# Performance work log

Measured on AMD Instinct MI355X. Metric: run time of the kernel, lower is better.

Reference implementation:

```python
import jax, jax.numpy as jnp
import numpy as np

H = 1024
B, S = 4, 2048
SCALE = 1.0 / np.sqrt(H)  # single-head: head_dim == hidden_dim


def setup_inputs() -> dict:
    key = jax.random.key(0)
    k1, k2, k3, k4 = jax.random.split(key, 4)
    inp = jax.random.normal(k1, (B, S, H), dtype=jnp.float32)
    # nn.Linear(h, h, bias=False) weights, stored [out, in]
    wq = jax.random.normal(k2, (H, H), dtype=jnp.float32) / np.sqrt(H)
    wk = jax.random.normal(k3, (H, H), dtype=jnp.float32) / np.sqrt(H)
    wv = jax.random.normal(k4, (H, H), dtype=jnp.float32) / np.sqrt(H)
    # causal mask, broadcast over batch: 1 = attend, 0 = masked
    attention_mask = jnp.broadcast_to(
        jnp.tril(jnp.ones((S, S), dtype=jnp.int32)), (B, S, S))
    return {"input": inp, "attention_mask": attention_mask,
            "wq": wq, "wk": wk, "wv": wv}


def reference(input, attention_mask, wq, wk, wv):
    # Linear: x @ W^T
    Q = jnp.einsum('bsh,oh->bso', input, wq)
    K = jnp.einsum('bsh,oh->bso', input, wk)
    V = jnp.einsum('bsh,oh->bso', input, wv)
    scores = jnp.einsum('bqh,bkh->bqk', Q, K) * SCALE  # [B,S,S]
    neg_inf = jnp.asarray(-jnp.inf, dtype=scores.dtype)
    scores = jnp.where(attention_mask == 0, neg_inf, scores)
    attn = jax.nn.softmax(scores, axis=-1)
    # dropout prob = 0.0 (eval): identity
    return jnp.einsum('bqk,bkh->bqh', attn, V)
```

## Files before the change

### kernel.cpp

```cpp
#include <hip/hip_runtime.h>
#include <hip/hip_bf16.h>
#include <stdint.h>

typedef __attribute__((ext_vector_type(8))) short short8;
typedef __attribute__((ext_vector_type(4))) float f32x4;
typedef __attribute__((ext_vector_type(4))) float fvec4;
typedef __attribute__((ext_vector_type(4))) unsigned short us4;

#define DEV static __device__ __forceinline__

constexpr int Hn = 1024;
constexpr int Bn = 4;
constexpr int Sn = 2048;
constexpr float SCALE_F = 0.03125f;
constexpr float LOG2E_F = 1.4426950408889634f;
constexpr float CEXP = SCALE_F * LOG2E_F;

DEV unsigned short f2bf(float f) {
  union { float f; unsigned u; } c; c.f = f;
  unsigned r = c.u + 0x7fffu + ((c.u >> 16) & 1u);
  return (unsigned short)(r >> 16);
}

DEV float bf2f(unsigned short b) {
  union { unsigned u; float f; } c; c.u = ((unsigned)b) << 16;
  return c.f;
}

DEV void gload16(const void* g, void* l) {
  __builtin_amdgcn_global_load_lds(
      (const __attribute__((address_space(1))) void*)g,
      (__attribute__((address_space(3))) void*)l, 16, 0, 0);
}

__global__ __launch_bounds__(256) void cvt_kernel(
    const float* __restrict__ x, const float* __restrict__ wq,
    const float* __restrict__ wk, const float* __restrict__ wv,
    unsigned short* __restrict__ xb, unsigned short* __restrict__ wb) {
  const int NX4 = Bn * Sn * Hn / 4;
  const int NW4 = Hn * Hn / 4;
  const int total = NX4 + 3 * NW4;
  for (int i = blockIdx.x * 256 + threadIdx.x; i < total; i += gridDim.x * 256) {
    const fvec4* s; us4* d; int j;
    if (i < NX4)                { s = (const fvec4*)x;  d = (us4*)xb;             j = i; }
    else if (i < NX4 + NW4)     { s = (const fvec4*)wq; d = (us4*)wb;             j = i - NX4; }
    else if (i < NX4 + 2 * NW4) { s = (const fvec4*)wk; d = (us4*)(wb + Hn * Hn); j = i - NX4 - NW4; }
    else                        { s = (const fvec4*)wv; d = (us4*)(wb + 2 * Hn * Hn); j = i - NX4 - 2 * NW4; }
    fvec4 v = s[j];
    us4 o;
    o[0] = f2bf(v[0]); o[1] = f2bf(v[1]); o[2] = f2bf(v[2]); o[3] = f2bf(v[3]);
    d[j] = o;
  }
}

__global__ __launch_bounds__(256) void gemm_bt_dbuf_kernel(
    const unsigned short* __restrict__ A, int lda,
    const unsigned short* __restrict__ Bm, int ldb,
    unsigned short* __restrict__ C0, unsigned short* __restrict__ C1,
    int n_split, int ldc, int bm_mask, int bm_shift, int K) {
  __shared__ __attribute__((aligned(16))) unsigned short As[2][128 * 32];
  __shared__ __attribute__((aligned(16))) unsigned short Bs[2][128 * 32];
  const int tid = threadIdx.x, lane = tid & 63, wave = tid >> 6;
  const int wr = wave >> 1, wc = wave & 1;
  const int q8 = gridDim.x >> 3;
  const int wgid = (blockIdx.x & 7) * q8 + (blockIdx.x >> 3);
  const int bm = wgid & bm_mask, bn = wgid >> bm_shift;

  const unsigned short* Ag = A + (int64_t)(bm * 128 + wave * 32 + (lane >> 2)) * lda + (lane & 3) * 8;
  const unsigned short* Bg = Bm + (int64_t)(bn * 128 + wave * 32 + (lane >> 2)) * ldb + (lane & 3) * 8;

  f32x4 zero = {0.f, 0.f, 0.f, 0.f};
  f32x4 acc[4][4];
#pragma unroll
  for (int m = 0; m < 4; m++)
#pragma unroll
    for (int n = 0; n < 4; n++) acc[m][n] = zero;

  auto stage = [&](int kt, int buf) {
    const int k0 = kt << 5;
    char* a = (char*)As[buf] + wave * 2048;
    char* b = (char*)Bs[buf] + wave * 2048;
    gload16(Ag + k0, a);
    gload16(Ag + k0 + 16 * lda, a + 1024);
    gload16(Bg + k0, b);
    gload16(Bg + k0 + 16 * ldb, b + 1024);
  };

  const int nkt = K >> 5;
  stage(0, 0);
  __syncthreads();
  for (int kt = 0; kt < nkt; ++kt) {
    const int buf = kt & 1;
    if (kt + 1 < nkt) stage(kt + 1, buf ^ 1);
    const short* Ap = (const short*)As[buf];
    const short* Bp = (const short*)Bs[buf];
    const int ko = (lane >> 4) * 8;
    short8 af[4], bfv[4];
#pragma unroll
    for (int m = 0; m < 4; m++)
      af[m] = *(const short8*)(Ap + (wr * 64 + m * 16 + (lane & 15)) * 32 + ko);
#pragma unroll
    for (int n = 0; n < 4; n++)
      bfv[n] = *(const short8*)(Bp + (wc * 64 + n * 16 + (lane & 15)) * 32 + ko);
#pragma unroll
    for (int m = 0; m < 4; m++)
#pragma unroll
      for (int n = 0; n < 4; n++)
        acc[m][n] = __builtin_amdgcn_mfma_f32_16x16x32_bf16(af[m], bfv[n], acc[m][n], 0, 0, 0);
    __syncthreads();
  }

#pragma unroll
  for (int n = 0; n < 4; n++) {
    int cc = bn * 128 + wc * 64 + n * 16;
    unsigned short* cb = C0;
    if (cc >= n_split) { cb = C1; cc -= n_split; }
    cc += (lane & 15);
#pragma unroll
    for (int m = 0; m < 4; m++) {
      const int r0 = bm * 128 + wr * 64 + m * 16 + ((lane >> 4) << 2);
#pragma unroll
      for (int j = 0; j < 4; j++)
        cb[(int64_t)(r0 + j) * ldc + cc] = f2bf(acc[m][n][j]);
    }
  }
}

__global__ __launch_bounds__(256) void scores_exp_kernel(
    const unsigned short* __restrict__ Qb, const unsigned short* __restrict__ Kbuf,
    unsigned short* __restrict__ P, int64_t p_zstride, int b0) {
  const int q8 = gridDim.x >> 3;
  const int wgid = (blockIdx.x & 7) * q8 + (blockIdx.x >> 3);
  const int zl = wgid / 136;
  const int t = wgid - zl * 136;
  int bm = (int)((sqrtf(8.f * t + 1.f) - 1.f) * 0.5f);
  if (bm * (bm + 1) / 2 > t) bm--;
  if ((bm + 1) * (bm + 2) / 2 <= t) bm++;
  const int bn = t - bm * (bm + 1) / 2;

  const int b = b0 + zl;
  const unsigned short* A = Qb + (int64_t)b * Sn * Hn;
  const unsigned short* Bm = Kbuf + (int64_t)b * Sn * Hn;
  unsigned short* C = P + (int64_t)zl * p_zstride;

  __shared__ __attribute__((aligned(16))) unsigned short As[2][128 * 32];
  __shared__ __attribute__((aligned(16))) unsigned short Bs[2][128 * 32];
  const int tid = threadIdx.x, lane = tid & 63, wave = tid >> 6;
  const int wr = wave >> 1, wc = wave & 1;

  const unsigned short* Ag = A + (int64_t)(bm * 128 + wave * 32 + (lane >> 2)) * Hn + (lane & 3) * 8;
  const unsigned short* Bg = Bm + (int64_t)(bn * 128 + wave * 32 + (lane >> 2)) * Hn + (lane & 3) * 8;

  f32x4 zero = {0.f, 0.f, 0.f, 0.f};
  f32x4 acc[4][4];
#pragma unroll
  for (int m = 0; m < 4; m++)
#pragma unroll
    for (int n = 0; n < 4; n++) acc[m][n] = zero;

  auto stage = [&](int kt, int buf) {
    const int k0 = kt << 5;
    char* a = (char*)As[buf] + wave * 2048;
    char* b2 = (char*)Bs[buf] + wave * 2048;
    gload16(Ag + k0, a);
    gload16(Ag + k0 + 16 * Hn, a + 1024);
    gload16(Bg + k0, b2);
    gload16(Bg + k0 + 16 * Hn, b2 + 1024);
  };

  stage(0, 0);
  __syncthreads();
  for (int kt = 0; kt < (Hn >> 5); ++kt) {
    const int buf = kt & 1;
    if (kt + 1 < (Hn >> 5)) stage(kt + 1, buf ^ 1);
    const short* Ap = (const short*)As[buf];
    const short* Bp = (const short*)Bs[buf];
    const int ko = (lane >> 4) * 8;
    short8 af[4], bfv[4];
#pragma unroll
    for (int m = 0; m < 4; m++)
      af[m] = *(const short8*)(Ap + (wr * 64 + m * 16 + (lane & 15)) * 32 + ko);
#pragma unroll
    for (int n = 0; n < 4; n++)
      bfv[n] = *(const short8*)(Bp + (wc * 64 + n * 16 + (lane & 15)) * 32 + ko);
#pragma unroll
    for (int m = 0; m < 4; m++)
#pragma unroll
      for (int n = 0; n < 4; n++)
        acc[m][n] = __builtin_amdgcn_mfma_f32_16x16x32_bf16(af[m], bfv[n], acc[m][n], 0, 0, 0);
    __syncthreads();
  }

#pragma unroll
  for (int n = 0; n < 4; n++) {
    const int cc = bn * 128 + wc * 64 + n * 16 + (lane & 15);
#pragma unroll
    for (int m = 0; m < 4; m++) {
      const int r0 = bm * 128 + wr * 64 + m * 16 + ((lane >> 4) << 2);
#pragma unroll
      for (int j = 0; j < 4; j++) {
        const int row = r0 + j;
        const float p = (cc <= row) ? __builtin_amdgcn_exp2f(acc[m][n][j] * CEXP) : 0.f;
        C[(int64_t)row * Sn + cc] = f2bf(p);
      }
    }
  }
}

__global__ __launch_bounds__(256) void rowsum_kernel(
    const unsigned short* __restrict__ P, float* __restrict__ l, int b0, int nb) {
  const int lane = threadIdx.x & 63, wave = threadIdx.x >> 6;
  const int r = blockIdx.x * 4 + wave;
  if (r >= nb * Sn) return;
  const int bl = r >> 11;
  const int q = r & (Sn - 1);
  const unsigned short* Pr = P + (int64_t)bl * Sn * Sn + (int64_t)q * Sn;
  float s = 0.f;
  for (int base = lane * 8; base < Sn; base += 512) {
    const int rem = q + 1 - base;
    if (rem <= 0) continue;
    short8 v = *(const short8*)(Pr + base);
#pragma unroll
    for (int e = 0; e < 8; ++e)
      if (e < rem) s += bf2f((unsigned short)v[e]);
  }
#pragma unroll
  for (int m = 1; m < 64; m <<= 1) s += __shfl_xor(s, m);
  if (lane == 0) l[(int64_t)(b0 + bl) * Sn + q] = s;
}

__global__ __launch_bounds__(256) void pv_gemm_kernel(
    const unsigned short* __restrict__ P, int64_t p_zstride,
    const unsigned short* __restrict__ VTb,
    const float* __restrict__ l,
    float* __restrict__ Out, int b0, int nb) {
  const int per_bm = 8 * nb;
  const int w = blockIdx.x;
  const int bm = 15 - (w / per_bm);
  const int inner = w - (15 - bm) * per_bm;
  const int bn = inner & 7;
  const int zl = inner >> 3;
  const int b = b0 + zl;

  __shared__ __attribute__((aligned(16))) unsigned short As[2][128 * 32];
  __shared__ __attribute__((aligned(16))) unsigned short Bs[2][128 * 32];
  const int tid = threadIdx.x, lane = tid & 63, wave = tid >> 6;
  const int wr = wave >> 1, wc = wave & 1;

  const unsigned short* A = P + (int64_t)zl * p_zstride;
  const unsigned short* Ag = A + (int64_t)(bm * 128 + wave * 32 + (lane >> 2)) * Sn + (lane & 3) * 8;
  const unsigned short* Bg = VTb + (int64_t)(bn * 128 + wave * 32 + (lane >> 2)) * (Bn * Sn)
                             + (int64_t)b * Sn + (lane & 3) * 8;

  f32x4 zero = {0.f, 0.f, 0.f, 0.f};
  f32x4 acc[4][4];
#pragma unroll
  for (int m = 0; m < 4; m++)
#pragma unroll
    for (int n = 0; n < 4; n++) acc[m][n] = zero;

  auto stage = [&](int kt, int buf) {
    const int k0 = kt << 5;
    char* a = (char*)As[buf] + wave * 2048;
    char* b2 = (char*)Bs[buf] + wave * 2048;
    gload16(Ag + k0, a);
    gload16(Ag + k0 + 16 * Sn, a + 1024);
    gload16(Bg + k0, b2);
    gload16(Bg + k0 + (int64_t)16 * (Bn * Sn), b2 + 1024);
  };

  const int nkt = (bm + 1) * 4;
  stage(0, 0);
  __syncthreads();
  for (int kt = 0; kt < nkt; ++kt) {
    const int buf = kt & 1;
    if (kt + 1 < nkt) stage(kt + 1, buf ^ 1);
    const short* Ap = (const short*)As[buf];
    const short* Bp = (const short*)Bs[buf];
    const int ko = (lane >> 4) * 8;
    short8 af[4], bfv[4];
#pragma unroll
    for (int m = 0; m < 4; m++)
      af[m] = *(const short8*)(Ap + (wr * 64 + m * 16 + (lane & 15)) * 32 + ko);
#pragma unroll
    for (int n = 0; n < 4; n++)
      bfv[n] = *(const short8*)(Bp + (wc * 64 + n * 16 + (lane & 15)) * 32 + ko);
#pragma unroll
    for (int m = 0; m < 4; m++)
#pragma unroll
      for (int n = 0; n < 4; n++)
        acc[m][n] = __builtin_amdgcn_mfma_f32_16x16x32_bf16(af[m], bfv[n], acc[m][n], 0, 0, 0);
    __syncthreads();
  }

#pragma unroll
  for (int m = 0; m < 4; m++) {
    const int r0 = bm * 128 + wr * 64 + m * 16 + ((lane >> 4) << 2);
#pragma unroll
    for (int j = 0; j < 4; j++) {
      const int q = r0 + j;
      const float linv = 1.0f / l[(int64_t)b * Sn + q];
#pragma unroll
      for (int n = 0; n < 4; n++) {
        const int d = bn * 128 + wc * 64 + n * 16 + (lane & 15);
        Out[(int64_t)b * Sn * Hn + (int64_t)q * Hn + d] = acc[m][n][j] * linv;
      }
    }
  }
}

extern "C" void kernel_launch(void* const* d_in, const int* in_sizes, int n_in,
                              void* d_out, int out_size, void* d_ws, size_t ws_size,
                              hipStream_t stream) {
  const float* x  = (const float*)d_in[0];
  const float* wq = (const float*)d_in[2];
  const float* wk = (const float*)d_in[3];
  const float* wv = (const float*)d_in[4];
  float* out = (float*)d_out;
  char* ws = (char*)d_ws;

  const int64_t MiB = 1ll << 20;
  unsigned short* xb = (unsigned short*)(ws);
  unsigned short* wb = (unsigned short*)(ws + 16 * MiB);
  float* l           = (float*)(ws + 22 * MiB);
  unsigned short* Qb = (unsigned short*)(ws + 23 * MiB);
  unsigned short* Kb = (unsigned short*)(ws + 39 * MiB);
  unsigned short* VT = (unsigned short*)(ws + 55 * MiB);
  unsigned short* P  = (unsigned short*)(ws + 71 * MiB);

  cvt_kernel<<<2048, 256, 0, stream>>>(x, wq, wk, wv, xb, wb);
  gemm_bt_dbuf_kernel<<<1024, 256, 0, stream>>>(
      xb, 1024, wb, 1024, Qb, Kb, 1024, 1024, 63, 6, 1024);
  gemm_bt_dbuf_kernel<<<512, 256, 0, stream>>>(
      wb + 2 * 1024 * 1024, 1024, xb, 1024, VT, VT, 1 << 30, 8192, 7, 3, 1024);

  int nb = 1;
  if (ws_size >= 103ull * MiB) nb = 4;
  else if (ws_size >= 87ull * MiB) nb = 2;
  for (int b0 = 0; b0 < Bn; b0 += nb) {
    scores_exp_kernel<<<136 * nb, 256, 0, stream>>>(
        Qb, Kb, P, (int64_t)Sn * Sn, b0);
    rowsum_kernel<<<nb * 512, 256, 0, stream>>>(P, l, b0, nb);
    pv_gemm_kernel<<<16 * 8 * nb, 256, 0, stream>>>(
        P, (int64_t)Sn * Sn, VT, l, out, b0, nb);
  }
}
```

Measured before the change: 179.6 us.

## Replace 128x128 GEMM kernels with a unified 256x256-tile MFMA kernel using swizzled LDS

Replaces the projection GEMM and the causal scores+exp kernel with one templated kernel. It uses 256x256 output tiles, 512 threads, a K-step of 64 and XOR-swizzled LDS layout to avoid bank conflicts. It also adds explicit s_barrier/vmcnt double-buffer synchronisation, setprio around the MFMA bursts, and a remainder-aware XCD block swizzle. The larger tiles raise data reuse per LDS/global load. The cost is far fewer workgroups (128–256 per launch on a 256-CU part), 128KB of LDS per block, and more wasted work on diagonal causal tiles.

Measured after the change: 181.6 us. Within noise of the previous version (+1.1%).

```diff
diff --git a/kernel.cpp b/kernel.cpp
--- a/kernel.cpp
+++ b/kernel.cpp
@@ -31,6 +31,13 @@
   __builtin_amdgcn_global_load_lds(
       (const __attribute__((address_space(1))) void*)g,
       (__attribute__((address_space(3))) void*)l, 16, 0, 0);
+}
+
+DEV void hw_barrier() { asm volatile("s_barrier" ::: "memory"); }
+
+DEV int swz_wg(int bid, int n) {
+  const int q = n >> 3, r = n & 7, x = bid & 7, o = bid >> 3;
+  return (x < r ? x * (q + 1) : r * (q + 1) + (x - r) * q) + o;
 }
 
 __global__ __launch_bounds__(256) void cvt_kernel(
@@ -53,155 +60,136 @@
   }
 }
 
-__global__ __launch_bounds__(256) void gemm_bt_dbuf_kernel(
-    const unsigned short* __restrict__ A, int lda,
-    const unsigned short* __restrict__ Bm, int ldb,
+template <int MODE>
+__global__ __launch_bounds__(512, 2) void gemm256_kernel(
+    const unsigned short* __restrict__ A, int lda, int64_t a_bstride,
+    const unsigned short* __restrict__ Bm, int ldb, int64_t b_bstride,
     unsigned short* __restrict__ C0, unsigned short* __restrict__ C1,
-    int n_split, int ldc, int bm_mask, int bm_shift, int K) {
-  __shared__ __attribute__((aligned(16))) unsigned short As[2][128 * 32];
-  __shared__ __attribute__((aligned(16))) unsigned short Bs[2][128 * 32];
+    int n_split, int ldc, int64_t c_bstride, int bm_mod, int K) {
+  __shared__ __attribute__((aligned(16))) unsigned short LA[2][256 * 64];
+  __shared__ __attribute__((aligned(16))) unsigned short LB[2][256 * 64];
   const int tid = threadIdx.x, lane = tid & 63, wave = tid >> 6;
-  const int wr = wave >> 1, wc = wave & 1;
-  const int q8 = gridDim.x >> 3;
-  const int wgid = (blockIdx.x & 7) * q8 + (blockIdx.x >> 3);
-  const int bm = wgid & bm_mask, bn = wgid >> bm_shift;
-
-  const unsigned short* Ag = A + (int64_t)(bm * 128 + wave * 32 + (lane >> 2)) * lda + (lane & 3) * 8;
-  const unsigned short* Bg = Bm + (int64_t)(bn * 128 + wave * 32 + (lane >> 2)) * ldb + (lane & 3) * 8;
+  const int wr = wave >> 2, wc = wave & 3;
+
+  int bm, bn;
+  const unsigned short* Ab = A;
+  const unsigned short* Bb = Bm;
+  unsigned short* Cb = C0;
+  if (MODE == 0) {
+    const int wg = swz_wg(blockIdx.x, gridDim.x);
+    bm = wg % bm_mod;
+    bn = wg / bm_mod;
+  } else {
+    const int wg = swz_wg(blockIdx.x, gridDim.x);
+    const int zl = wg / 36;
+    const int t = wg - zl * 36;
+    bm = (int)((sqrtf(8.f * t + 1.f) - 1.f) * 0.5f);
+    if (bm * (bm + 1) / 2 > t) bm--;
+    if ((bm + 1) * (bm + 2) / 2 <= t) bm++;
+    bn = t - bm * (bm + 1) / 2;
+    Ab += (int64_t)zl * a_bstride;
+    Bb += (int64_t)zl * b_bstride;
+    Cb += (int64_t)zl * c_bstride;
+  }
+
+  const int srow = wave * 32 + (lane >> 3);
+  const int scol = (((lane & 7) ^ (lane >> 3)) << 3);
+  const unsigned short* AgS = Ab + (int64_t)(bm * 256 + srow) * lda + scol;
+  const unsigned short* BgS = Bb + (int64_t)(bn * 256 + srow) * ldb + scol;
 
   f32x4 zero = {0.f, 0.f, 0.f, 0.f};
-  f32x4 acc[4][4];
-#pragma unroll
-  for (int m = 0; m < 4; m++)
+  f32x4 acc[8][4];
+#pragma unroll
+  for (int m = 0; m < 8; m++)
 #pragma unroll
     for (int n = 0; n < 4; n++) acc[m][n] = zero;
 
-  auto stage = [&](int kt, int buf) {
-    const int k0 = kt << 5;
-    char* a = (char*)As[buf] + wave * 2048;
-    char* b = (char*)Bs[buf] + wave * 2048;
-    gload16(Ag + k0, a);
-    gload16(Ag + k0 + 16 * lda, a + 1024);
-    gload16(Bg + k0, b);
-    gload16(Bg + k0 + 16 * ldb, b + 1024);
+  auto stage = [&](int t, int buf) {
+    char* la = (char*)LA[buf] + wave * 4096;
+    char* lb = (char*)LB[buf] + wave * 4096;
+    const int k0 = t << 6;
+#pragma unroll
+    for (int j = 0; j < 4; ++j) {
+      gload16(AgS + (int64_t)(j * 8) * lda + k0, la + j * 1024);
+      gload16(BgS + (int64_t)(j * 8) * ldb + k0, lb + j * 1024);
+    }
   };
 
-  const int nkt = K >> 5;
+  const int nkt = K >> 6;
+  const int ln15 = lane & 15;
+  const int hi = (lane >> 4) * 16;
+  const int sw = (ln15 & 7) << 4;
+
   stage(0, 0);
-  __syncthreads();
-  for (int kt = 0; kt < nkt; ++kt) {
-    const int buf = kt & 1;
-    if (kt + 1 < nkt) stage(kt + 1, buf ^ 1);
-    const short* Ap = (const short*)As[buf];
-    const short* Bp = (const short*)Bs[buf];
-    const int ko = (lane >> 4) * 8;
-    short8 af[4], bfv[4];
-#pragma unroll
-    for (int m = 0; m < 4; m++)
-      af[m] = *(const short8*)(Ap + (wr * 64 + m * 16 + (lane & 15)) * 32 + ko);
-#pragma unroll
-    for (int n = 0; n < 4; n++)
-      bfv[n] = *(const short8*)(Bp + (wc * 64 + n * 16 + (lane & 15)) * 32 + ko);
-#pragma unroll
-    for (int m = 0; m < 4; m++)
-#pragma unroll
-      for (int n = 0; n < 4; n++)
-        acc[m][n] = __builtin_amdgcn_mfma_f32_16x16x32_bf16(af[m], bfv[n], acc[m][n], 0, 0, 0);
-    __syncthreads();
-  }
-
-#pragma unroll
-  for (int n = 0; n < 4; n++) {
-    int cc = bn * 128 + wc * 64 + n * 16;
-    unsigned short* cb = C0;
-    if (cc >= n_split) { cb = C1; cc -= n_split; }
-    cc += (lane & 15);
-#pragma unroll
-    for (int m = 0; m < 4; m++) {
-      const int r0 = bm * 128 + wr * 64 + m * 16 + ((lane >> 4) << 2);
-#pragma unroll
-      for (int j = 0; j < 4; j++)
-        cb[(int64_t)(r0 + j) * ldc + cc] = f2bf(acc[m][n][j]);
-    }
-  }
-}
-
-__global__ __launch_bounds__(256) void scores_exp_kernel(
-    const unsigned short* __restrict__ Qb, const unsigned short* __restrict__ Kbuf,
-    unsigned short* __restrict__ P, int64_t p_zstride, int b0) {
-  const int q8 = gridDim.x >> 3;
-  const int wgid = (blockIdx.x & 7) * q8 + (blockIdx.x >> 3);
-  const int zl = wgid / 136;
-  const int t = wgid - zl * 136;
-  int bm = (int)((sqrtf(8.f * t + 1.f) - 1.f) * 0.5f);
-  if (bm * (bm + 1) / 2 > t) bm--;
-  if ((bm + 1) * (bm + 2) / 2 <= t) bm++;
-  const int bn = t - bm * (bm + 1) / 2;
-
-  const int b = b0 + zl;
-  const unsigned short* A = Qb + (int64_t)b * Sn * Hn;
-  const unsigned short* Bm = Kbuf + (int64_t)b * Sn * Hn;
-  unsigned short* C = P + (int64_t)zl * p_zstride;
-
-  __shared__ __attribute__((aligned(16))) unsigned short As[2][128 * 32];
-  __shared__ __attribute__((aligned(16))) unsigned short Bs[2][128 * 32];
-  const int tid = threadIdx.x, lane = tid & 63, wave = tid >> 6;
-  const int wr = wave >> 1, wc = wave & 1;
-
-  const unsigned short* Ag = A + (int64_t)(bm * 128 + wave * 32 + (lane >> 2)) * Hn + (lane & 3) * 8;
-  const unsigned short* Bg = Bm + (int64_t)(bn * 128 + wave * 32 + (lane >> 2)) * Hn + (lane & 3) * 8;
-
-  f32x4 zero = {0.f, 0.f, 0.f, 0.f};
-  f32x4 acc[4][4];
-#pragma unroll
-  for (int m = 0; m < 4; m++)
-#pragma unroll
-    for (int n = 0; n < 4; n++) acc[m][n] = zero;
-
-  auto stage = [&](int kt, int buf) {
-    const int k0 = kt << 5;
-    char* a = (char*)As[buf] + wave * 2048;
-    char* b2 = (char*)Bs[buf] + wave * 2048;
-    gload16(Ag + k0, a);
-    gload16(Ag + k0 + 16 * Hn, a + 1024);
-    gload16(Bg + k0, b2);
-    gload16(Bg + k0 + 16 * Hn, b2 + 1024);
-  };
-
-  stage(0, 0);
-  __syncthreads();
-  for (int kt = 0; kt < (Hn >> 5); ++kt) {
-    const int buf = kt & 1;
-    if (kt + 1 < (Hn >> 5)) stage(kt + 1, buf ^ 1);
-    const short* Ap = (const short*)As[buf];
-    const short* Bp = (const short*)Bs[buf];
-    const int ko = (lane >> 4) * 8;
-    short8 af[4], bfv[4];
-#pragma unroll
-    for (int m = 0; m < 4; m++)
-      af[m] = *(const short8*)(Ap + (wr * 64 + m * 16 + (lane & 15)) * 32 + ko);
-#pragma unroll
-    for (int n = 0; n < 4; n++)
-      bfv[n] = *(const short8*)(Bp + (wc * 64 + n * 16 + (lane & 15)) * 32 + ko);
-#pragma unroll
-    for (int m = 0; m < 4; m++)
-#pragma unroll
-      for (int n = 0; n < 4; n++)
-        acc[m][n] = __builtin_amdgcn_mfma_f32_16x16x32_bf16(af[m], bfv[n], acc[m][n], 0, 0, 0);
-    __syncthreads();
-  }
-
-#pragma unroll
-  for (int n = 0; n < 4; n++) {
-    const int cc = bn * 128 + wc * 64 + n * 16 + (lane & 15);
-#pragma unroll
-    for (int m = 0; m < 4; m++) {
-      const int r0 = bm * 128 + wr * 64 + m * 16 + ((lane >> 4) << 2);
-#pragma unroll
-      for (int j = 0; j < 4; j++) {
-        const int row = r0 + j;
-        const float p = (cc <= row) ? __builtin_amdgcn_exp2f(acc[m][n][j] * CEXP) : 0.f;
-        C[(int64_t)row * Sn + cc] = f2bf(p);
+  for (int t = 0; t < nkt; ++t) {
+    const int buf = t & 1;
+    hw_barrier();
+    if (t + 1 < nkt) {
+      stage(t + 1, buf ^ 1);
+      asm volatile("s_waitcnt vmcnt(8)" ::: "memory");
+    } else {
+      asm volatile("s_waitcnt vmcnt(0)" ::: "memory");
+    }
+    hw_barrier();
+    __builtin_amdgcn_sched_barrier(0);
+
+    const char* la = (const char*)LA[buf];
+    const char* lb = (const char*)LB[buf];
+#pragma unroll
+    for (int qm = 0; qm < 2; ++qm) {
+#pragma unroll
+      for (int ks = 0; ks < 2; ++ks) {
+        const int kb = (ks * 64 + hi) ^ sw;
+        short8 a[4];
+#pragma unroll
+        for (int fr = 0; fr < 4; ++fr)
+          a[fr] = *(const short8*)(la + (wr * 128 + qm * 64 + fr * 16 + ln15) * 128 + kb);
+#pragma unroll
+        for (int qn = 0; qn < 2; ++qn) {
+          short8 b0 = *(const short8*)(lb + (wc * 64 + qn * 32 + ln15) * 128 + kb);
+          short8 b1 = *(const short8*)(lb + (wc * 64 + qn * 32 + 16 + ln15) * 128 + kb);
+          __builtin_amdgcn_s_setprio(1);
+#pragma unroll
+          for (int fr = 0; fr < 4; ++fr) {
+            acc[qm * 4 + fr][qn * 2 + 0] =
+                __builtin_amdgcn_mfma_f32_16x16x32_bf16(a[fr], b0, acc[qm * 4 + fr][qn * 2 + 0], 0, 0, 0);
+            acc[qm * 4 + fr][qn * 2 + 1] =
+                __builtin_amdgcn_mfma_f32_16x16x32_bf16(a[fr], b1, acc[qm * 4 + fr][qn * 2 + 1], 0, 0, 0);
+          }
+          __builtin_amdgcn_s_setprio(0);
+        }
+      }
+    }
+  }
+
+  if (MODE == 0) {
+#pragma unroll
+    for (int n = 0; n < 4; n++) {
+      int cc = bn * 256 + wc * 64 + n * 16;
+      unsigned short* cb = Cb;
+      if (cc >= n_split) { cb = C1; cc -= n_split; }
+      cc += ln15;
+#pragma unroll
+      for (int m = 0; m < 8; m++) {
+        const int r0 = bm * 256 + wr * 128 + m * 16 + ((lane >> 4) << 2);
+#pragma unroll
+        for (int j = 0; j < 4; j++)
+          cb[(int64_t)(r0 + j) * ldc + cc] = f2bf(acc[m][n][j]);
+      }
+    }
+  } else {
+#pragma unroll
+    for (int n = 0; n < 4; n++) {
+      const int cc = bn * 256 + wc * 64 + n * 16 + ln15;
+#pragma unroll
+      for (int m = 0; m < 8; m++) {
+        const int r0 = bm * 256 + wr * 128 + m * 16 + ((lane >> 4) << 2);
+#pragma unroll
+        for (int j = 0; j < 4; j++) {
+          const int row = r0 + j;
+          const float p = (cc <= row) ? __builtin_amdgcn_exp2f(acc[m][n][j] * CEXP) : 0.f;
+          Cb[(int64_t)row * ldc + cc] = f2bf(p);
+        }
       }
     }
   }
@@ -329,17 +317,19 @@
   unsigned short* P  = (unsigned short*)(ws + 71 * MiB);
 
   cvt_kernel<<<2048, 256, 0, stream>>>(x, wq, wk, wv, xb, wb);
-  gemm_bt_dbuf_kernel<<<1024, 256, 0, stream>>>(
-      xb, 1024, wb, 1024, Qb, Kb, 1024, 1024, 63, 6, 1024);
-  gemm_bt_dbuf_kernel<<<512, 256, 0, stream>>>(
-      wb + 2 * 1024 * 1024, 1024, xb, 1024, VT, VT, 1 << 30, 8192, 7, 3, 1024);
+  gemm256_kernel<0><<<256, 512, 0, stream>>>(
+      xb, 1024, 0, wb, 1024, 0, Qb, Kb, 1024, 1024, 0, 32, 1024);
+  gemm256_kernel<0><<<128, 512, 0, stream>>>(
+      wb + 2 * 1024 * 1024, 1024, 0, xb, 1024, 0, VT, VT, 1 << 30, 8192, 0, 4, 1024);
 
   int nb = 1;
   if (ws_size >= 103ull * MiB) nb = 4;
   else if (ws_size >= 87ull * MiB) nb = 2;
   for (int b0 = 0; b0 < Bn; b0 += nb) {
-    scores_exp_kernel<<<136 * nb, 256, 0, stream>>>(
-        Qb, Kb, P, (int64_t)Sn * Sn, b0);
+    gemm256_kernel<1><<<36 * nb, 512, 0, stream>>>(
+        Qb + (int64_t)b0 * Sn * Hn, 1024, (int64_t)Sn * Hn,
+        Kb + (int64_t)b0 * Sn * Hn, 1024, (int64_t)Sn * Hn,
+        P, nullptr, 1 << 30, Sn, (int64_t)Sn * Sn, 8, 1024);
     rowsum_kernel<<<nb * 512, 256, 0, stream>>>(P, l, b0, nb);
     pv_gemm_kernel<<<16 * 8 * nb, 256, 0, stream>>>(
         P, (int64_t)Sn * Sn, VT, l, out, b0, nb);
```
